# Performance work log

Measured on AMD Instinct MI355X. Metric: run time of the kernel, lower is better.

## Reference

```python
import jax, jax.numpy as jnp
import numpy as np

NUM_HEADS = 8


def setup_inputs() -> dict:
    key = jax.random.key(0)
    k0, k1, k2 = jax.random.split(key, 3)
    B, C, D, H, W = 2, 256, 16, 16, 8
    x = jax.random.normal(k0, (B, C, D, H, W), dtype=jnp.float32)
    # 1x1x1 Conv3d weights are pointwise linear maps over channels
    w_qkv = jax.random.normal(k1, (3 * C, C), dtype=jnp.float32) * 0.02
    b_qkv = jnp.zeros((3 * C,), dtype=jnp.float32)
    w_out = jax.random.normal(k2, (C, C), dtype=jnp.float32) * 0.02
    b_out = jnp.zeros((C,), dtype=jnp.float32)
    return {"x": x, "w_qkv": w_qkv, "b_qkv": b_qkv, "w_out": w_out, "b_out": b_out}


def reference(x, w_qkv, b_qkv, w_out, b_out):
    b, c, d, h, w = x.shape
    nh = NUM_HEADS
    hd = c // nh
    scale = hd ** (-0.5)
    n = d * h * w
    xf = x.reshape(b, c, n)  # flatten spatial volume to N tokens
    # to_qkv: pointwise conv == channel-mixing matmul
    qkv = jnp.einsum('oc,bcn->bon', w_qkv, xf) + b_qkv[None, :, None]
    # torch: view(b, H, 3*hd, N) then chunk(3, dim=2) -> per-head channel grouping
    qkv = qkv.reshape(b, nh, 3 * hd, n)
    q, k, v = jnp.split(qkv, 3, axis=2)  # each (b, nh, hd, n)
    sim = jnp.einsum('bhcn,bhcm->bhnm', q, k) * scale  # (b, nh, N, N)
    attn = jax.nn.softmax(sim, axis=-1)
    out = jnp.einsum('bhnm,bhcm->bhcn', attn, v)  # (b, nh, hd, N)
    out = out.reshape(b, c, n)
    out = jnp.einsum('oc,bcn->bon', w_out, out) + b_out[None, :, None]
    return x + out.reshape(b, c, d, h, w)
```

## Files before the change

kernel.cpp:

```cpp
#include <hip/hip_runtime.h>
#include <hip/hip_bf16.h>
#include <math.h>

#define BB 2
#define CC 256
#define NH 8
#define HD 32
#define NN 2048
#define KSPAN 1024
#define QBLK 64
#define KTILE 64
#define NITER (KSPAN / KTILE)
#define QK_SCALE 0.25500917f

typedef __attribute__((ext_vector_type(8))) short short8;
typedef __attribute__((ext_vector_type(8))) unsigned short ushort8;
typedef __attribute__((ext_vector_type(4))) float f32x4;

__device__ inline unsigned short f2bf(float f) {
    __hip_bfloat16 h = __float2bfloat16(f);
    return __builtin_bit_cast(unsigned short, h);
}
__device__ inline int kperm(int k) {
    return 32 * (k >> 5) + 16 * ((k >> 2) & 1) + 4 * ((k >> 3) & 3) + (k & 3);
}
__device__ inline int xcd_chunk(int orig, int nwg) {
    int q = nwg >> 3, r = nwg & 7, x = orig & 7, s = orig >> 3;
    return (x < r ? x * (q + 1) : r * (q + 1) + (x - r) * q) + s;
}

__global__ __launch_bounds__(256) void qkv_mfma(const float* __restrict__ x,
                                                const float* __restrict__ wq,
                                                const float* __restrict__ bias,
                                                unsigned short* __restrict__ qt,
                                                unsigned short* __restrict__ ktt,
                                                unsigned short* __restrict__ vt) {
    const int l = xcd_chunk(blockIdx.x, 768);
    const int m0 = (l % 12) * 64;
    const int xtile = l / 12;
    const int n0 = (xtile & 31) * 64;
    const int b = xtile >> 5;
    const int t = threadIdx.x, lane = t & 63, wid = t >> 6;
    const int g = lane >> 4, ln = lane & 15;
    __shared__ __align__(16) unsigned short Aw[4][64][36];
    __shared__ __align__(16) unsigned short Bx[4][64][36];
    f32x4 acc[4] = {};

    const int sm = t & 63, sch = t >> 6;
    const int pc = t >> 4, pn = t & 15;
    const int c0 = pc * 8, nl = pn * 4;
    const float* xb = x + (size_t)b * CC * NN + n0;

    for (int kh = 0; kh < 2; ++kh) {
        __syncthreads();
        {
            const float* wsrc = wq + (size_t)(m0 + sm) * CC + kh * 128 + sch * 32;
            float wv[32];
#pragma unroll
            for (int j = 0; j < 8; ++j) *(float4*)&wv[j * 4] = *(const float4*)&wsrc[j * 4];
#pragma unroll
            for (int j2 = 0; j2 < 4; ++j2) {
                ushort8 p;
#pragma unroll
                for (int e = 0; e < 8; ++e) p[e] = f2bf(wv[j2 * 8 + e]);
                *(ushort8*)&Aw[sch][sm][j2 * 8] = p;
            }
        }
        {
            const float* xsrc = xb + (size_t)(kh * 128 + c0) * NN + nl;
            float xv[8][4];
#pragma unroll
            for (int i = 0; i < 8; ++i) *(float4*)&xv[i][0] = *(const float4*)&xsrc[(size_t)i * NN];
#pragma unroll
            for (int i2 = 0; i2 < 4; ++i2) {
                ushort8 p;
#pragma unroll
                for (int e = 0; e < 8; ++e) p[e] = f2bf(xv[e][i2]);
                *(ushort8*)&Bx[pc >> 2][nl + i2][(pc & 3) * 8] = p;
            }
        }
        __syncthreads();
#pragma unroll
        for (int ks = 0; ks < 4; ++ks) {
            short8 aW = *(const short8*)&Aw[ks][wid * 16 + ln][g * 8];
#pragma unroll
            for (int nt = 0; nt < 4; ++nt) {
                short8 bX = *(const short8*)&Bx[ks][nt * 16 + ln][g * 8];
                acc[nt] = __builtin_amdgcn_mfma_f32_16x16x32_bf16(aW, bX, acc[nt], 0, 0, 0);
            }
        }
    }
    const int obase = m0 + wid * 16 + 4 * g;
    const int sect = obase % 96;
    const int type = sect >> 5;
    const int head = obase / 96;
    const int cb4 = obase & 31;
    float bv[4];
#pragma unroll
    for (int r = 0; r < 4; ++r) bv[r] = bias[obase + r];
    if (type == 2) {
#pragma unroll
        for (int nt = 0; nt < 4; ++nt) {
            int n = n0 + nt * 16 + ln;
#pragma unroll
            for (int r = 0; r < 4; ++r)
                vt[((size_t)(b * NH + head) * HD + cb4 + r) * NN + n] = f2bf(acc[nt][r] + bv[r]);
        }
    } else {
        const float sc = (type == 0) ? QK_SCALE : 1.0f;
        unsigned short* dst = (type == 0) ? qt : ktt;
#pragma unroll
        for (int nt = 0; nt < 4; ++nt) {
            int n = n0 + nt * 16 + ln;
            ushort4 r4;
            r4.x = f2bf((acc[nt][0] + bv[0]) * sc);
            r4.y = f2bf((acc[nt][1] + bv[1]) * sc);
            r4.z = f2bf((acc[nt][2] + bv[2]) * sc);
            r4.w = f2bf((acc[nt][3] + bv[3]) * sc);
            *(ushort4*)&dst[((size_t)(b * NH + head) * NN + n) * HD + cb4] = r4;
        }
    }
}

__global__ __launch_bounds__(512) void attn_mfma(const unsigned short* __restrict__ Qt,
                                                 const unsigned short* __restrict__ Kt,
                                                 const unsigned short* __restrict__ Vt,
                                                 unsigned short* __restrict__ aout_t) {
    const int l = xcd_chunk(blockIdx.x, 512);
    const int n0 = (l & 31) * QBLK;
    const int bh = l >> 5;
    const int h = bh & 7, b = bh >> 3;
    const int t = threadIdx.x;
    const int lane = t & 63, wid = t >> 6;
    const int g = lane >> 4, ln = lane & 15;
    const int qg = wid & 3, whalf = wid >> 2;

    __shared__ __align__(16) unsigned short Qs[QBLK][40];
    __shared__ __align__(16) unsigned short Ks[2][2][KTILE][40];
    __shared__ __align__(16) unsigned short Vs[2][2][HD][72];

    const unsigned short* qb = Qt + ((size_t)(b * NH + h) * NN + n0) * HD;
    const unsigned short* kb = Kt + (size_t)(b * NH + h) * NN * HD;
    const unsigned short* vb = Vt + (size_t)(b * NH + h) * HD * NN;

    if (t < 256) {
        int q = t >> 2, ch = (t & 3) * 8;
        *(ushort8*)&Qs[q][ch] = *(const ushort8*)&qb[(size_t)q * HD + ch];
    }
    __syncthreads();
    const short8 bQ = *(const short8*)&Qs[qg * 16 + ln][g * 8];

    const int th = t & 255, sthalf = t >> 8;
    const int sk = th >> 2, sch = (th & 3) * 8;
    const int rowK = kperm(sk);
    const int vcc = th >> 3, vn = (th & 7) * 8;
    const size_t hbase = (size_t)sthalf * KSPAN;

    ushort8 kpre, vpre;
    kpre = *(const ushort8*)&kb[(hbase + sk) * HD + sch];
    vpre = *(const ushort8*)&vb[(size_t)vcc * NN + hbase + vn];

    float m_run = -1e30f, l_run = 0.f;
    f32x4 oacc[2];
    const f32x4 zero4 = {0.f, 0.f, 0.f, 0.f};
    oacc[0] = zero4; oacc[1] = zero4;

    for (int it = 0; it < NITER; ++it) {
        const int buf = it & 1;
        *(ushort8*)&Ks[sthalf][buf][rowK][sch] = kpre;
        *(ushort8*)&Vs[sthalf][buf][vcc][vn]   = vpre;
        if (it + 1 < NITER) {
            size_t kt = hbase + (size_t)(it + 1) * KTILE;
            kpre = *(const ushort8*)&kb[(kt + sk) * HD + sch];
            vpre = *(const ushort8*)&vb[(size_t)vcc * NN + kt + vn];
        }
        __syncthreads();

        f32x4 sacc[4];
        __builtin_amdgcn_s_setprio(1);
#pragma unroll
        for (int t8 = 0; t8 < 4; ++t8) {
            short8 aK = *(const short8*)&Ks[whalf][buf][t8 * 16 + ln][g * 8];
            sacc[t8] = __builtin_amdgcn_mfma_f32_16x16x32_bf16(aK, bQ, zero4, 0, 0, 0);
        }
        __builtin_amdgcn_s_setprio(0);

        float mx[4];
#pragma unroll
        for (int t8 = 0; t8 < 4; ++t8)
            mx[t8] = fmaxf(fmaxf(sacc[t8][0], sacc[t8][1]), fmaxf(sacc[t8][2], sacc[t8][3]));
        float tmax = fmaxf(fmaxf(mx[0], mx[1]), fmaxf(mx[2], mx[3]));
        tmax = fmaxf(tmax, __shfl_xor(tmax, 16));
        tmax = fmaxf(tmax, __shfl_xor(tmax, 32));
        if (!__all(tmax <= m_run + 8.0f)) {
            float mnew = fmaxf(m_run, tmax);
            float rsc = exp2f(m_run - mnew);
            m_run = mnew;
            l_run *= rsc;
#pragma unroll
            for (int r = 0; r < 4; ++r) {
                float rr = __shfl(rsc, 4 * g + r);
                oacc[0][r] *= rr;
                oacc[1][r] *= rr;
            }
        }
#pragma unroll
        for (int t8 = 0; t8 < 4; ++t8) {
            sacc[t8][0] = exp2f(sacc[t8][0] - m_run);
            sacc[t8][1] = exp2f(sacc[t8][1] - m_run);
            sacc[t8][2] = exp2f(sacc[t8][2] - m_run);
            sacc[t8][3] = exp2f(sacc[t8][3] - m_run);
        }
        float ps[4];
#pragma unroll
        for (int t8 = 0; t8 < 4; ++t8)
            ps[t8] = (sacc[t8][0] + sacc[t8][1]) + (sacc[t8][2] + sacc[t8][3]);
        float lsum = (ps[0] + ps[1]) + (ps[2] + ps[3]);
        lsum += __shfl_xor(lsum, 16);
        lsum += __shfl_xor(lsum, 32);
        l_run += lsum;

        short8 aP[2];
#pragma unroll
        for (int kc = 0; kc < 2; ++kc)
#pragma unroll
            for (int u = 0; u < 2; ++u)
#pragma unroll
                for (int r = 0; r < 4; ++r)
                    aP[kc][u * 4 + r] = (short)f2bf(sacc[2 * kc + u][r]);

        __builtin_amdgcn_s_setprio(1);
#pragma unroll
        for (int kc = 0; kc < 2; ++kc) {
            short8 bV0 = *(const short8*)&Vs[whalf][buf][ln][kc * 32 + g * 8];
            short8 bV1 = *(const short8*)&Vs[whalf][buf][16 + ln][kc * 32 + g * 8];
            oacc[0] = __builtin_amdgcn_mfma_f32_16x16x32_bf16(aP[kc], bV0, oacc[0], 0, 0, 0);
            oacc[1] = __builtin_amdgcn_mfma_f32_16x16x32_bf16(aP[kc], bV1, oacc[1], 0, 0, 0);
        }
        __builtin_amdgcn_s_setprio(0);
    }

    __syncthreads();
    float*  Of  = (float*)&Ks[0][0][0][0];
    float2* MLs = (float2*)&Vs[0][0][0][0];
#pragma unroll
    for (int ct = 0; ct < 2; ++ct)
#pragma unroll
        for (int r = 0; r < 4; ++r)
            Of[((whalf * 64) + qg * 16 + 4 * g + r) * 40 + ct * 16 + ln] = oacc[ct][r];
    if (g == 0) MLs[whalf * 64 + qg * 16 + ln] = make_float2(m_run, l_run);
    __syncthreads();
    {
        const int q = t >> 3, c0 = (t & 7) * 4;
        f32x4 o0 = *(const f32x4*)&Of[(size_t)q * 40 + c0];
        f32x4 o1 = *(const f32x4*)&Of[(size_t)(64 + q) * 40 + c0];
        float2 ml0 = MLs[q], ml1 = MLs[64 + q];
        float M = fmaxf(ml0.x, ml1.x);
        float w0 = exp2f(ml0.x - M), w1 = exp2f(ml1.x - M);
        float dinv = 1.0f / (w0 * ml0.y + w1 * ml1.y);
        w0 *= dinv; w1 *= dinv;
        ushort4 r4;
        r4.x = f2bf(w0 * o0[0] + w1 * o1[0]);
        r4.y = f2bf(w0 * o0[1] + w1 * o1[1]);
        r4.z = f2bf(w0 * o0[2] + w1 * o1[2]);
        r4.w = f2bf(w0 * o0[3] + w1 * o1[3]);
        *(ushort4*)&aout_t[((size_t)b * NN + n0 + q) * CC + h * HD + c0] = r4;
    }
}

__global__ __launch_bounds__(256) void proj_mfma(const unsigned short* __restrict__ aout_t,
                                                 const float* __restrict__ wo,
                                                 const float* __restrict__ bias,
                                                 const float* __restrict__ x,
                                                 float* __restrict__ out) {
    const int l = xcd_chunk(blockIdx.x, 512);
    const int n0 = (l & 63) * 32;
    const int bm = l >> 6;
    const int m0 = (bm & 3) * 64, b = bm >> 2;
    const int t = threadIdx.x, lane = t & 63, wid = t >> 6;
    const int g = lane >> 4, ln = lane & 15;
    __shared__ __align__(16) unsigned short Aw[4][64][36];
    __shared__ __align__(16) unsigned short Bx[4][32][36];
    f32x4 acc[2] = {};
    const unsigned short* ab = aout_t + ((size_t)b * NN + n0) * CC;

    const int sm = t & 63, sch = t >> 6;
    const int bn = t & 31, bch = t >> 5;
    for (int kh = 0; kh < 2; ++kh) {
        __syncthreads();
        {
            const float* wsrc = wo + (size_t)(m0 + sm) * CC + kh * 128 + sch * 32;
            float wv[32];
#pragma unroll
            for (int j = 0; j < 8; ++j) *(float4*)&wv[j * 4] = *(const float4*)&wsrc[j * 4];
#pragma unroll
            for (int j2 = 0; j2 < 4; ++j2) {
                ushort8 p;
#pragma unroll
                for (int e = 0; e < 8; ++e) p[e] = f2bf(wv[j2 * 8 + e]);
                *(ushort8*)&Aw[sch][sm][j2 * 8] = p;
            }
        }
        {
            int ks = bch >> 1, off = (bch & 1) * 16;
            const unsigned short* src = &ab[(size_t)bn * CC + kh * 128 + ks * 32 + off];
            *(ushort8*)&Bx[ks][bn][off]     = *(const ushort8*)&src[0];
            *(ushort8*)&Bx[ks][bn][off + 8] = *(const ushort8*)&src[8];
        }
        __syncthreads();
#pragma unroll
        for (int ks = 0; ks < 4; ++ks) {
            short8 aW = *(const short8*)&Aw[ks][wid * 16 + ln][g * 8];
#pragma unroll
            for (int nt = 0; nt < 2; ++nt) {
                short8 bX = *(const short8*)&Bx[ks][nt * 16 + ln][g * 8];
                acc[nt] = __builtin_amdgcn_mfma_f32_16x16x32_bf16(aW, bX, acc[nt], 0, 0, 0);
            }
        }
    }
    const int mbase = m0 + wid * 16 + 4 * g;
    float bv[4];
#pragma unroll
    for (int r = 0; r < 4; ++r) bv[r] = bias[mbase + r];
#pragma unroll
    for (int nt = 0; nt < 2; ++nt) {
        int n = n0 + nt * 16 + ln;
#pragma unroll
        for (int r = 0; r < 4; ++r) {
            size_t off = ((size_t)b * CC + mbase + r) * NN + n;
            out[off] = acc[nt][r] + bv[r] + x[off];
        }
    }
}

extern "C" void kernel_launch(void* const* d_in, const int* in_sizes, int n_in,
                              void* d_out, int out_size, void* d_ws, size_t ws_size,
                              hipStream_t stream) {
    const float* x     = (const float*)d_in[0];
    const float* w_qkv = (const float*)d_in[1];
    const float* b_qkv = (const float*)d_in[2];
    const float* w_out = (const float*)d_in[3];
    const float* b_out = (const float*)d_in[4];
    float* out = (float*)d_out;

    unsigned short* qt     = (unsigned short*)d_ws;
    unsigned short* ktt    = qt  + (size_t)BB * NH * NN * HD;
    unsigned short* vt     = ktt + (size_t)BB * NH * NN * HD;
    unsigned short* aout_t = vt  + (size_t)BB * NH * NN * HD;

    qkv_mfma<<<dim3(768), 256, 0, stream>>>(x, w_qkv, b_qkv, qt, ktt, vt);
    attn_mfma<<<dim3(512), 512, 0, stream>>>(qt, ktt, vt, aout_t);
    proj_mfma<<<dim3(512), 256, 0, stream>>>(aout_t, w_out, b_out, x, out);
}
```

Baseline: 53.05 us.

## Stage QKV epilogue through LDS for coalesced stores; deepen attention K/V prefetch

The QKV projection epilogue now writes bf16 results into shared memory, reusing the input tile buffers, and then emits 16-byte coalesced global stores for Q, K and V. Before, V used scattered 2-byte stores and Q/K used 8-byte stores. In the attention kernel, the K/V register prefetch now runs two tiles ahead, with the loop unrolled by two and a lambda for the tile compute. This adds extra syncs and LDS traffic in the projection, and more live registers in attention, which could lower occupancy.

```diff
diff --git a/kernel.cpp b/kernel.cpp
--- a/kernel.cpp
+++ b/kernel.cpp
@@ -90,34 +90,47 @@
             }
         }
     }
-    const int obase = m0 + wid * 16 + 4 * g;
-    const int sect = obase % 96;
-    const int type = sect >> 5;
-    const int head = obase / 96;
-    const int cb4 = obase & 31;
-    float bv[4];
-#pragma unroll
-    for (int r = 0; r < 4; ++r) bv[r] = bias[obase + r];
-    if (type == 2) {
-#pragma unroll
-        for (int nt = 0; nt < 4; ++nt) {
-            int n = n0 + nt * 16 + ln;
-#pragma unroll
-            for (int r = 0; r < 4; ++r)
-                vt[((size_t)(b * NH + head) * HD + cb4 + r) * NN + n] = f2bf(acc[nt][r] + bv[r]);
-        }
-    } else {
-        const float sc = (type == 0) ? QK_SCALE : 1.0f;
-        unsigned short* dst = (type == 0) ? qt : ktt;
-#pragma unroll
-        for (int nt = 0; nt < 4; ++nt) {
-            int n = n0 + nt * 16 + ln;
-            ushort4 r4;
-            r4.x = f2bf((acc[nt][0] + bv[0]) * sc);
-            r4.y = f2bf((acc[nt][1] + bv[1]) * sc);
-            r4.z = f2bf((acc[nt][2] + bv[2]) * sc);
-            r4.w = f2bf((acc[nt][3] + bv[3]) * sc);
-            *(ushort4*)&dst[((size_t)(b * NH + head) * NN + n) * HD + cb4] = r4;
+    __syncthreads();
+    unsigned short (*Tqk)[64][40] = (unsigned short (*)[64][40])&Aw[0][0][0];
+    unsigned short (*Tv)[32][72]  = (unsigned short (*)[32][72])&Bx[0][0][0];
+    {
+        const int grp = wid >> 1;
+        const int cl0 = (wid & 1) * 16 + 4 * g;
+        const int gm0 = m0 + grp * 32;
+        const int gtype = (gm0 % 96) >> 5;
+        const float sc = (gtype == 0) ? QK_SCALE : 1.0f;
+        float bv[4];
+#pragma unroll
+        for (int r = 0; r < 4; ++r) bv[r] = bias[gm0 + cl0 + r];
+        if (gtype == 2) {
+#pragma unroll
+            for (int nt = 0; nt < 4; ++nt)
+#pragma unroll
+                for (int r = 0; r < 4; ++r)
+                    Tv[grp][cl0 + r][nt * 16 + ln] = f2bf(acc[nt][r] + bv[r]);
+        } else {
+#pragma unroll
+            for (int nt = 0; nt < 4; ++nt)
+#pragma unroll
+                for (int r = 0; r < 4; ++r)
+                    Tqk[grp][nt * 16 + ln][cl0 + r] = f2bf((acc[nt][r] + bv[r]) * sc);
+        }
+    }
+    __syncthreads();
+#pragma unroll
+    for (int grp2 = 0; grp2 < 2; ++grp2) {
+        const int gm = m0 + grp2 * 32;
+        const int gtype = (gm % 96) >> 5;
+        const int head = gm / 96;
+        if (gtype == 2) {
+            const int cl = t >> 3, n8 = (t & 7) * 8;
+            ushort8 v = *(const ushort8*)&Tv[grp2][cl][n8];
+            *(ushort8*)&vt[((size_t)(b * NH + head) * HD + cl) * NN + n0 + n8] = v;
+        } else {
+            unsigned short* dst = (gtype == 0) ? qt : ktt;
+            const int nr = t >> 2, c8 = (t & 3) * 8;
+            ushort8 v = *(const ushort8*)&Tqk[grp2][nr][c8];
+            *(ushort8*)&dst[((size_t)(b * NH + head) * NN + n0 + nr) * HD + c8] = v;
         }
     }
 }
@@ -156,26 +169,17 @@
     const int vcc = th >> 3, vn = (th & 7) * 8;
     const size_t hbase = (size_t)sthalf * KSPAN;
 
-    ushort8 kpre, vpre;
-    kpre = *(const ushort8*)&kb[(hbase + sk) * HD + sch];
-    vpre = *(const ushort8*)&vb[(size_t)vcc * NN + hbase + vn];
+    ushort8 kpreA = *(const ushort8*)&kb[(hbase + 0 * KTILE + sk) * HD + sch];
+    ushort8 vpreA = *(const ushort8*)&vb[(size_t)vcc * NN + hbase + 0 * KTILE + vn];
+    ushort8 kpreB = *(const ushort8*)&kb[(hbase + 1 * KTILE + sk) * HD + sch];
+    ushort8 vpreB = *(const ushort8*)&vb[(size_t)vcc * NN + hbase + 1 * KTILE + vn];
 
     float m_run = -1e30f, l_run = 0.f;
     f32x4 oacc[2];
     const f32x4 zero4 = {0.f, 0.f, 0.f, 0.f};
     oacc[0] = zero4; oacc[1] = zero4;
 
-    for (int it = 0; it < NITER; ++it) {
-        const int buf = it & 1;
-        *(ushort8*)&Ks[sthalf][buf][rowK][sch] = kpre;
-        *(ushort8*)&Vs[sthalf][buf][vcc][vn]   = vpre;
-        if (it + 1 < NITER) {
-            size_t kt = hbase + (size_t)(it + 1) * KTILE;
-            kpre = *(const ushort8*)&kb[(kt + sk) * HD + sch];
-            vpre = *(const ushort8*)&vb[(size_t)vcc * NN + kt + vn];
-        }
-        __syncthreads();
-
+    auto compute_tile = [&](int buf) {
         f32x4 sacc[4];
         __builtin_amdgcn_s_setprio(1);
 #pragma unroll
@@ -238,6 +242,27 @@
             oacc[1] = __builtin_amdgcn_mfma_f32_16x16x32_bf16(aP[kc], bV1, oacc[1], 0, 0, 0);
         }
         __builtin_amdgcn_s_setprio(0);
+    };
+
+    for (int it = 0; it < NITER; it += 2) {
+        *(ushort8*)&Ks[sthalf][0][rowK][sch] = kpreA;
+        *(ushort8*)&Vs[sthalf][0][vcc][vn]   = vpreA;
+        if (it + 2 < NITER) {
+            size_t kt = hbase + (size_t)(it + 2) * KTILE;
+            kpreA = *(const ushort8*)&kb[(kt + sk) * HD + sch];
+            vpreA = *(const ushort8*)&vb[(size_t)vcc * NN + kt + vn];
+        }
+        __syncthreads();
+        compute_tile(0);
+        *(ushort8*)&Ks[sthalf][1][rowK][sch] = kpreB;
+        *(ushort8*)&Vs[sthalf][1][vcc][vn]   = vpreB;
+        if (it + 3 < NITER) {
+            size_t kt = hbase + (size_t)(it + 3) * KTILE;
+            kpreB = *(const ushort8*)&kb[(kt + sk) * HD + sch];
+            vpreB = *(const ushort8*)&vb[(size_t)vcc * NN + kt + vn];
+        }
+        __syncthreads();
+        compute_tile(1);
     }
 
     __syncthreads();
```

New measurement: 51.73 us. -2.5%, faster.
